# Optimization experiments

Hardware: AMD Instinct MI355X
Metric: run time of the kernel (lower is better)

Reference implementation:

```python
import jax, jax.numpy as jnp
import numpy as np

K = 3  # kernel size along all four dims (kernel_size=3, padding=2=K-1, circular)


def setup_inputs() -> dict:
    key = jax.random.key(0)
    k1, k2, k3 = jax.random.split(key, 3)
    b, c_in, c_out, s = 4, 64, 64, 16
    x = jax.random.normal(k1, (b, c_in, s, s, s, s), dtype=jnp.float32)
    # torch grouped Conv3d weight (out_c*K, c_in, K, K, K) viewed as (K, out_c, c_in, K, K, K):
    # group g (= kernel slice along dim 0) uses weight[g].
    weight = jax.random.normal(k2, (K, c_out, c_in, K, K, K), dtype=jnp.float32) * 0.05
    bias = jax.random.normal(k3, (c_out,), dtype=jnp.float32)
    return {"x": x, "weight": weight, "bias": bias}


def _conv4d_circular(x, weight, bias):
    k = weight.shape[0]
    p = k - 1
    lo, hi = (p + 1) // 2, p // 2  # circular pad split used by do_padding
    b, c = x.shape[0], x.shape[1]
    s0, s1, s2, s3 = x.shape[2:]
    c_out = weight.shape[1]
    # circular-pad the three inner spatial dims only (dim s0 handled via rolls)
    xp = jnp.pad(x, ((0, 0), (0, 0), (0, 0), (lo, hi), (lo, hi), (lo, hi)), mode='wrap')
    # fold s0 into batch: (b*s0, c, S1, S2, S3)
    xr = xp.transpose(0, 2, 1, 3, 4, 5).reshape(b * s0, c, s1 + p, s2 + p, s3 + p)
    # grouped conv with input replicated across groups == k independent VALID 3D convs
    conv = lambda w: jax.lax.conv_general_dilated(
        xr, w, window_strides=(1, 1, 1), padding='VALID',
        dimension_numbers=('NCDHW', 'OIDHW', 'NCDHW'))
    out = jax.vmap(conv)(weight)  # (k, b*s0, c_out, s1, s2, s3)
    out = out.reshape(k, b, s0, c_out, s1, s2, s3).transpose(0, 1, 3, 2, 4, 5, 6)
    # combine kernel slices along dim-0 axis: result[..., t] = sum_i out[i, ..., (t+i) % s0]
    rolled = jnp.stack([jnp.roll(out[i], -i, axis=2) for i in range(k)], axis=0)
    res = rolled.sum(axis=0) + bias[None, :, None, None, None, None]
    shift = (p + 1) // 2  # math.ceil(padding[0] / 2)
    res = jnp.roll(res, shift, axis=2)
    return res  # (b, c_out, s0, s1, s2, s3)


def reference(x, weight, bias):
    return _conv4d_circular(x, weight, bias)
```

## Files before the change

### kernel.cpp

```cpp
#include <hip/hip_runtime.h>

typedef unsigned short u16;
typedef __attribute__((ext_vector_type(8))) __bf16 bf16x8;
typedef __attribute__((ext_vector_type(8))) short short8;
typedef __attribute__((ext_vector_type(4))) float floatx4;

__device__ __forceinline__ u16 f2bf(float f){
  unsigned int x = __float_as_uint(f);
  unsigned int r = (x + 0x7fffu + ((x >> 16) & 1u)) >> 16;
  return (u16)r;
}

__global__ void repack_w_kernel(const float* __restrict__ w, u16* __restrict__ wp){
  int idx = blockIdx.x * 256 + threadIdx.x;
  if (idx >= 81*64*64) return;
  int cw  = idx & 31;
  int t1  = idx >> 5;
  int co  = t1 & 63; t1 >>= 6;
  int kc  = t1 & 1;  t1 >>= 1;
  int tap = t1;
  int dw = tap % 3, dz = (tap/3) % 3, dy = (tap/9) % 3, dt = tap/27;
  int ci = kc*32 + cw;
  int in_idx = ((((dt*64 + co)*64 + ci)*3 + dy)*3 + dz)*3 + dw;
  wp[idx] = f2bf(w[in_idx]);
}

__global__ __launch_bounds__(256, 2) void conv4d_mfma_kernel(
    const float* __restrict__ x, const u16* __restrict__ wp,
    const float* __restrict__ bias, float* __restrict__ out)
{
  __shared__ __attribute__((aligned(16))) u16 x_lds[256*72];
  __shared__ __attribute__((aligned(16))) u16 a_lds[3*2*64*32];

  const int bx = blockIdx.x;
  const int y = bx & 15, t = (bx >> 4) & 15, b = bx >> 8;
  const int tid  = threadIdx.x;
  const int lane = tid & 63;
  const int wv   = tid >> 6;
  const int wl   = lane & 15;
  const int q    = lane >> 4;

  floatx4 acc[4][4];
#pragma unroll
  for (int zi = 0; zi < 4; ++zi)
#pragma unroll
    for (int mi = 0; mi < 4; ++mi)
      acc[zi][mi] = (floatx4)0.0f;

  const float* xb = x + (size_t)b * 64 * 65536;

  for (int dt = 0; dt < 3; ++dt){
    const int tt = (t + dt + 15) & 15;
    for (int dy = 0; dy < 3; ++dy){
      const int yy = (y + dy + 15) & 15;
      __syncthreads();
      {
        const float* src = xb + tt*4096 + yy*256 + tid;
#pragma unroll
        for (int oct = 0; oct < 8; ++oct){
          float v[8];
#pragma unroll
          for (int j = 0; j < 8; ++j)
            v[j] = src[(size_t)(oct*8 + j) * 65536];
          short8 vv;
#pragma unroll
          for (int j = 0; j < 8; ++j) vv[j] = (short)f2bf(v[j]);
          *(short8*)(x_lds + tid*72 + oct*8) = vv;
        }
      }
      for (int dz = 0; dz < 3; ++dz){
        const int tap0 = ((dt*3 + dy)*3 + dz)*3;
        __syncthreads();
        {
          const u16* asrc = wp + (size_t)tap0 * 4096;
#pragma unroll
          for (int i = 0; i < 6; ++i){
            int e = (i*256 + tid) * 8;
            *(short8*)(a_lds + e) = *(const short8*)(asrc + e);
          }
        }
        __syncthreads();
#pragma unroll
        for (int dw = 0; dw < 3; ++dw){
          const int ww = (wl + dw + 15) & 15;
#pragma unroll
          for (int kc = 0; kc < 2; ++kc){
            bf16x8 af[4];
#pragma unroll
            for (int mi = 0; mi < 4; ++mi)
              af[mi] = *(const bf16x8*)(a_lds + ((dw*2 + kc)*64 + mi*16 + wl)*32 + q*8);
#pragma unroll
            for (int zi = 0; zi < 4; ++zi){
              const int zz = (wv*4 + zi + dz + 15) & 15;
              bf16x8 bf = *(const bf16x8*)(x_lds + (zz*16 + ww)*72 + kc*32 + q*8);
#pragma unroll
              for (int mi = 0; mi < 4; ++mi)
                acc[zi][mi] = __builtin_amdgcn_mfma_f32_16x16x32_bf16(af[mi], bf, acc[zi][mi], 0, 0, 0);
            }
          }
        }
      }
    }
  }

  float bvals[4][4];
#pragma unroll
  for (int mi = 0; mi < 4; ++mi)
#pragma unroll
    for (int r = 0; r < 4; ++r)
      bvals[mi][r] = bias[mi*16 + q*4 + r];

  float* ob = out + (size_t)b * 64 * 65536 + t*4096 + y*256 + wl;
#pragma unroll
  for (int zi = 0; zi < 4; ++zi){
    const int z = wv*4 + zi;
#pragma unroll
    for (int mi = 0; mi < 4; ++mi){
#pragma unroll
      for (int r = 0; r < 4; ++r){
        const int co = mi*16 + q*4 + r;
        ob[(size_t)co*65536 + z*16] = acc[zi][mi][r] + bvals[mi][r];
      }
    }
  }
}

extern "C" void kernel_launch(void* const* d_in, const int* in_sizes, int n_in,
                              void* d_out, int out_size, void* d_ws, size_t ws_size,
                              hipStream_t stream) {
  const float* x    = (const float*)d_in[0];
  const float* w    = (const float*)d_in[1];
  const float* bias = (const float*)d_in[2];
  u16* wp    = (u16*)d_ws;
  float* out = (float*)d_out;

  repack_w_kernel<<<1296, 256, 0, stream>>>(w, wp);
  conv4d_mfma_kernel<<<1024, 256, 0, stream>>>(x, wp, bias, out);
}
```

Baseline: 265.0 us.

## Pre-convert input to bf16 planes and stream tiles via global_load_lds

```diff
diff --git a/kernel.cpp b/kernel.cpp
--- a/kernel.cpp
+++ b/kernel.cpp
@@ -9,6 +9,136 @@
   unsigned int x = __float_as_uint(f);
   unsigned int r = (x + 0x7fffu + ((x >> 16) & 1u)) >> 16;
   return (u16)r;
+}
+
+#define GLL(g, l) __builtin_amdgcn_global_load_lds( \
+    (const __attribute__((address_space(1))) void*)(g), \
+    (__attribute__((address_space(3))) void*)(l), 16, 0, 0)
+
+__global__ void prep_kernel(const float* __restrict__ x, const float* __restrict__ w,
+                            u16* __restrict__ xp, u16* __restrict__ wp){
+  const int bx = blockIdx.x;
+  const int tid = threadIdx.x;
+  if (bx < 1024){
+    const int y = bx & 15, t = (bx >> 4) & 15, b = bx >> 8;
+    const float* src = x + (size_t)b*64*65536 + t*4096 + y*256 + tid;
+    u16* dst = xp + (size_t)bx*16384 + tid*64;
+#pragma unroll
+    for (int oct = 0; oct < 8; ++oct){
+      float v[8];
+#pragma unroll
+      for (int j = 0; j < 8; ++j)
+        v[j] = src[(oct*8 + j)*65536];
+      short8 vv;
+#pragma unroll
+      for (int j = 0; j < 8; ++j) vv[j] = (short)f2bf(v[j]);
+      *(short8*)(dst + ((oct ^ (tid & 7))*8)) = vv;
+    }
+  } else {
+    int idx = (bx - 1024)*256 + tid;
+    if (idx < 81*64*64){
+      int r  = idx;
+      int dw = r % 3; r /= 3;
+      int dz = r % 3; r /= 3;
+      int dy = r % 3; r /= 3;
+      int ci = r & 63; r >>= 6;
+      int co = r & 63; r >>= 6;
+      int dt = r;
+      int tap = ((dt*3 + dy)*3 + dz)*3 + dw;
+      int kc = ci >> 5, ci32 = ci & 31;
+      wp[tap*4096 + kc*2048 + co*32 + ci32] = f2bf(w[idx]);
+    }
+  }
+}
+
+__global__ __launch_bounds__(256, 2) void conv4d_mfma_fast(
+    const u16* __restrict__ xp, const u16* __restrict__ wp,
+    const float* __restrict__ bias, float* __restrict__ out)
+{
+  __shared__ __attribute__((aligned(16))) u16 x_lds[16384];
+  __shared__ __attribute__((aligned(16))) u16 a_lds[12288];
+
+  const int bx = blockIdx.x;
+  const int y = bx & 15, t = (bx >> 4) & 15, b = bx >> 8;
+  const int tid  = threadIdx.x;
+  const int lane = tid & 63;
+  const int wv   = tid >> 6;
+  const int wl   = lane & 15;
+  const int q    = lane >> 4;
+
+  floatx4 acc[4][4];
+#pragma unroll
+  for (int zi = 0; zi < 4; ++zi)
+#pragma unroll
+    for (int mi = 0; mi < 4; ++mi)
+      acc[zi][mi] = (floatx4)0.0f;
+
+  for (int dt = 0; dt < 3; ++dt){
+    const int tt = (t + dt + 15) & 15;
+    for (int dy = 0; dy < 3; ++dy){
+      const int yy = (y + dy + 15) & 15;
+      __syncthreads();
+      {
+        const u16* plane = xp + (size_t)(((b*16 + tt)*16) + yy) * 16384;
+#pragma unroll
+        for (int i = 0; i < 8; ++i)
+          GLL(plane + wv*4096 + i*512 + lane*8, x_lds + wv*4096 + i*512);
+      }
+      for (int dz = 0; dz < 3; ++dz){
+        const int tap0 = ((dt*3 + dy)*3 + dz)*3;
+        __syncthreads();
+        {
+          const u16* asrc = wp + (size_t)tap0 * 4096;
+#pragma unroll
+          for (int i = 0; i < 6; ++i)
+            GLL(asrc + wv*3072 + i*512 + lane*8, a_lds + wv*3072 + i*512);
+        }
+        __syncthreads();
+#pragma unroll
+        for (int dw = 0; dw < 3; ++dw){
+          const int ww = (wl + dw + 15) & 15;
+          const int wx = ww & 7;
+#pragma unroll
+          for (int kc = 0; kc < 2; ++kc){
+            bf16x8 af[4];
+#pragma unroll
+            for (int mi = 0; mi < 4; ++mi)
+              af[mi] = *(const bf16x8*)(a_lds + ((dw*2 + kc)*64 + mi*16 + wl)*32 + q*8);
+            const int chunk = ((kc*4 + q) ^ wx)*8;
+#pragma unroll
+            for (int zi = 0; zi < 4; ++zi){
+              const int zz = (wv*4 + zi + dz + 15) & 15;
+              bf16x8 bf = *(const bf16x8*)(x_lds + (zz*16 + ww)*64 + chunk);
+#pragma unroll
+              for (int mi = 0; mi < 4; ++mi)
+                acc[zi][mi] = __builtin_amdgcn_mfma_f32_16x16x32_bf16(af[mi], bf, acc[zi][mi], 0, 0, 0);
+            }
+          }
+        }
+      }
+    }
+  }
+
+  float bvals[4][4];
+#pragma unroll
+  for (int mi = 0; mi < 4; ++mi)
+#pragma unroll
+    for (int r = 0; r < 4; ++r)
+      bvals[mi][r] = bias[mi*16 + q*4 + r];
+
+  float* ob = out + (size_t)b*64*65536 + t*4096 + y*256 + wl;
+#pragma unroll
+  for (int zi = 0; zi < 4; ++zi){
+    const int z = wv*4 + zi;
+#pragma unroll
+    for (int mi = 0; mi < 4; ++mi){
+#pragma unroll
+      for (int r = 0; r < 4; ++r){
+        const int co = mi*16 + q*4 + r;
+        ob[(size_t)co*65536 + z*16] = acc[zi][mi][r] + bvals[mi][r];
+      }
+    }
+  }
 }
 
 __global__ void repack_w_kernel(const float* __restrict__ w, u16* __restrict__ wp){
@@ -31,7 +161,6 @@
 {
   __shared__ __attribute__((aligned(16))) u16 x_lds[256*72];
   __shared__ __attribute__((aligned(16))) u16 a_lds[3*2*64*32];
-
   const int bx = blockIdx.x;
   const int y = bx & 15, t = (bx >> 4) & 15, b = bx >> 8;
   const int tid  = threadIdx.x;
@@ -39,16 +168,13 @@
   const int wv   = tid >> 6;
   const int wl   = lane & 15;
   const int q    = lane >> 4;
-
   floatx4 acc[4][4];
 #pragma unroll
   for (int zi = 0; zi < 4; ++zi)
 #pragma unroll
     for (int mi = 0; mi < 4; ++mi)
       acc[zi][mi] = (floatx4)0.0f;
-
   const float* xb = x + (size_t)b * 64 * 65536;
-
   for (int dt = 0; dt < 3; ++dt){
     const int tt = (t + dt + 15) & 15;
     for (int dy = 0; dy < 3; ++dy){
@@ -102,14 +228,12 @@
       }
     }
   }
-
   float bvals[4][4];
 #pragma unroll
   for (int mi = 0; mi < 4; ++mi)
 #pragma unroll
     for (int r = 0; r < 4; ++r)
       bvals[mi][r] = bias[mi*16 + q*4 + r];
-
   float* ob = out + (size_t)b * 64 * 65536 + t*4096 + y*256 + wl;
 #pragma unroll
   for (int zi = 0; zi < 4; ++zi){
@@ -131,9 +255,18 @@
   const float* x    = (const float*)d_in[0];
   const float* w    = (const float*)d_in[1];
   const float* bias = (const float*)d_in[2];
-  u16* wp    = (u16*)d_ws;
   float* out = (float*)d_out;
 
-  repack_w_kernel<<<1296, 256, 0, stream>>>(w, wp);
-  conv4d_mfma_kernel<<<1024, 256, 0, stream>>>(x, wp, bias, out);
-}
+  const size_t xp_bytes = (size_t)1024 * 16384 * 2;
+  const size_t wp_bytes = 81*64*64*2;
+  if (ws_size >= xp_bytes + wp_bytes){
+    u16* xp = (u16*)d_ws;
+    u16* wp = (u16*)((char*)d_ws + xp_bytes);
+    prep_kernel<<<1024 + 1296, 256, 0, stream>>>(x, w, xp, wp);
+    conv4d_mfma_fast<<<1024, 256, 0, stream>>>(xp, wp, bias, out);
+  } else {
+    u16* wp = (u16*)d_ws;
+    repack_w_kernel<<<1296, 256, 0, stream>>>(w, wp);
+    conv4d_mfma_kernel<<<1024, 256, 0, stream>>>(x, wp, bias, out);
+  }
+}
```

Result: no change. 261.9 us (-1.2%).
